# Kernel tuning notes

Hardware: AMD Instinct MI355X
Metric: run time of the kernel (lower is better)

## Reference

```python
import jax, jax.numpy as jnp
import numpy as np

F = 32          # num_features
E = 20          # size_of_expansion
CUTOFF = 5.0
N, K = 30000, 32  # nodes x dense neighbors


def cosine_cutoff(d, cutoff):
    # 0.5*(cos(pi*d/cutoff)+1) for d < cutoff, else 0
    return jnp.where(d < cutoff, 0.5 * (jnp.cos(jnp.pi * d / cutoff) + 1.0), 0.0)


def setup_inputs() -> dict:
    key = jax.random.key(0)
    ks = jax.random.split(key, 12)
    s = jax.random.normal(ks[0], (N, K, 1, F), jnp.float32)
    v = jax.random.normal(ks[1], (N, K, 3, F), jnp.float32)
    expansion = jax.random.normal(ks[2], (N, K, E), jnp.float32)
    direction = jax.random.normal(ks[3], (N, K, 3), jnp.float32)
    mask = (jax.random.uniform(ks[4], (N, K, 1)) > 0.2).astype(jnp.float32)
    edge_distance = jax.random.uniform(ks[5], (N, K, 1), jnp.float32) * (1.2 * CUTOFF)
    sc1 = 1.0 / np.sqrt(F)
    sc2 = 1.0 / np.sqrt(E)
    W1 = jax.random.uniform(ks[6], (F, F), jnp.float32, -sc1, sc1)
    b1 = jax.random.uniform(ks[7], (F,), jnp.float32, -sc1, sc1)
    W2 = jax.random.uniform(ks[8], (F, 3 * F), jnp.float32, -sc1, sc1)
    b2 = jax.random.uniform(ks[9], (3 * F,), jnp.float32, -sc1, sc1)
    Wr = jax.random.uniform(ks[10], (E, 3 * F), jnp.float32, -sc2, sc2)
    br = jax.random.uniform(ks[11], (3 * F,), jnp.float32, -sc2, sc2)
    return dict(s=s, v=v, expansion=expansion, direction=direction, mask=mask,
                edge_distance=edge_distance, W1=W1, b1=b1, W2=W2, b2=b2, Wr=Wr, br=br)


def reference(s, v, expansion, direction, mask, edge_distance, W1, b1, W2, b2, Wr, br):
    # msg_left: Linear -> SiLU -> Linear, on s [N,K,1,F] -> [N,K,1,3F]
    left_mul = jax.nn.silu(s @ W1 + b1) @ W2 + b2
    # msg_right: Linear on expansion [N,K,E] -> [N,K,3F] -> [N,K,1,3F]
    right_pre = (expansion @ Wr + br)[..., None, :]
    f_cut = cosine_cutoff(edge_distance, CUTOFF)[..., None]     # [N,K,1,1]
    gated = left_mul * (right_pre * f_cut)                      # [N,K,1,3F]
    a, b, c = jnp.split(gated, 3, axis=-1)                      # each [N,K,1,F]
    mask_ = mask[..., None]                                     # [N,K,1,1]
    delta_s = jnp.sum(mask_ * b, axis=-3)                       # [N,1,F]
    delta_v = jnp.sum(mask_ * (v * a + direction[..., None] * c), axis=-3)  # [N,3,F]
    return (delta_s, delta_v)
```

## Files before the change

kernel.cpp:

```cpp
#include <hip/hip_runtime.h>
#include <hip/hip_bf16.h>

typedef __attribute__((ext_vector_type(8))) short bf16x8;
typedef __attribute__((ext_vector_type(4))) float f32x4;

#define GSTR 68

__device__ __forceinline__ short f2bf(float f) {
  unsigned u = __float_as_uint(f);
  u += 0x7fffu + ((u >> 16) & 1u);
  return (short)(u >> 16);
}

__device__ __forceinline__ bf16x8 cvt8(float4 A, float4 B) {
  union { bf16x8 v; __hip_bfloat162 h[4]; } u;
  u.h[0] = __float22bfloat162_rn(make_float2(A.x, A.y));
  u.h[1] = __float22bfloat162_rn(make_float2(A.z, A.w));
  u.h[2] = __float22bfloat162_rn(make_float2(B.x, B.y));
  u.h[3] = __float22bfloat162_rn(make_float2(B.z, B.w));
  return u.v;
}

__device__ __forceinline__ bf16x8 ldsfrag(const int4* p) {
  union { int4 i; bf16x8 b; } u;
  u.i = *p;
  return u.b;
}

__device__ __forceinline__ float silu_(float x) {
  return __fdividef(x, 1.f + __expf(-x));
}

__global__ void pack_weights_kernel(
    const float* __restrict__ W1, const float* __restrict__ W2,
    const float* __restrict__ WR, const float* __restrict__ BR,
    int4* __restrict__ wsf)
{
  const int tid = threadIdx.x, wid = tid >> 6, l = tid & 63;
  const int col16 = l & 15, c = l >> 4, kc = c << 3;
  for (int t = wid; t < 14; t += 4) {
    int q[4];
    #pragma unroll
    for (int jj = 0; jj < 4; ++jj) {
      float f0, f1;
      if (t < 2) {
        int k0 = kc + 2*jj;
        int co = (t << 4) + col16;
        f0 = W1[k0*32 + co]; f1 = W1[(k0+1)*32 + co];
      } else if (t < 8) {
        int j0 = 2*jj;
        int feat = (j0 < 4) ? (4*c + j0) : (16 + 4*c + (j0 - 4));
        int co = ((t-2) << 4) + col16;
        f0 = W2[feat*96 + co]; f1 = W2[(feat+1)*96 + co];
      } else {
        int k0 = kc + 2*jj;
        int co = ((t-8) << 4) + col16;
        f0 = (k0   < 20) ? WR[k0*96 + co]     : ((k0   == 20) ? BR[co] : 0.f);
        f1 = (k0+1 < 20) ? WR[(k0+1)*96 + co] : ((k0+1 == 20) ? BR[co] : 0.f);
      }
      q[jj] = ((int)(unsigned short)f2bf(f0)) |
              (((int)(unsigned short)f2bf(f1)) << 16);
    }
    wsf[t*64 + l] = make_int4(q[0], q[1], q[2], q[3]);
  }
}

__global__ __launch_bounds__(256, 3) void deepdft_v9(
    const float* __restrict__ S, const float* __restrict__ V,
    const float* __restrict__ EXPN, const float* __restrict__ DIR,
    const float* __restrict__ MASK, const float* __restrict__ DIST,
    const float* __restrict__ B1, const float* __restrict__ B2,
    const int4* __restrict__ wsf,
    float* __restrict__ OUT, int n_nodes)
{
  __shared__ int4  wlds[14][64];
  __shared__ float glds[4][16 * GSTR];

  const int tid = threadIdx.x, wid = tid >> 6, l = tid & 63;
  const int col16 = l & 15, c = l >> 4, kc = c << 3;
  const int er8 = l >> 2, fo = l & 3;

  int n = blockIdx.x * 4 + wid;
  if (n >= n_nodes) n = n_nodes - 1;
  const int eb0 = n << 5, eb1 = eb0 + 16;

  float dv0 = DIST[eb0 + col16];
  float mv0 = MASK[eb0 + col16];
  float dv1 = DIST[eb1 + col16];
  float mv1 = MASK[eb1 + col16];
  float drv = DIR[(size_t)eb0 * 3 + (l < 48 ? l : 47)];

  #pragma unroll
  for (int t = wid; t < 14; t += 4) wlds[t][l] = wsf[t*64 + l];

  f32x4 b1a, b1b;
  {
    float4 t0 = *reinterpret_cast<const float4*>(B1 + 4*c);
    float4 t1 = *reinterpret_cast<const float4*>(B1 + 16 + 4*c);
    b1a[0]=t0.x; b1a[1]=t0.y; b1a[2]=t0.z; b1a[3]=t0.w;
    b1b[0]=t1.x; b1b[1]=t1.y; b1b[2]=t1.z; b1b[3]=t1.w;
  }
  float b2v[6];
  #pragma unroll
  for (int t = 0; t < 6; ++t) b2v[t] = B2[(t << 4) + col16];

  float wvl0 = 0.f, wvl1 = 0.f;
  if (dv0 < 5.f) wvl0 = mv0 * 0.5f * (__cosf(0.62831853071795865f * dv0) + 1.f);
  if (dv1 < 5.f) wvl1 = mv1 * 0.5f * (__cosf(0.62831853071795865f * dv1) + 1.f);

  const float4 z4 = make_float4(0.f, 0.f, 0.f, 0.f);
  float4 sS0 = z4, sS1 = z4, sE0 = z4;
  float4 sE1 = (c == 2) ? make_float4(1.f, 0.f, 0.f, 0.f) : z4;
  float4 vva[6];
  #pragma unroll
  for (int j = 0; j < 6; ++j) vva[j] = z4;

  auto issueS = [&](int eb) {
    const float* sp = S + (size_t)(eb + col16) * 32 + kc;
    sS0 = *reinterpret_cast<const float4*>(sp);
    sS1 = *reinterpret_cast<const float4*>(sp + 4);
    const float* ep = EXPN + (size_t)(eb + col16) * 20;
    if (c < 2) {
      sE0 = *reinterpret_cast<const float4*>(ep + kc);
      sE1 = *reinterpret_cast<const float4*>(ep + kc + 4);
    } else if (c == 2) {
      sE0 = *reinterpret_cast<const float4*>(ep + 16);
    }
  };
  auto issueV = [&](int eb) {
    const float* vb = V + (size_t)(eb + er8) * 96 + fo * 8;
    vva[0] = *reinterpret_cast<const float4*>(vb);
    vva[1] = *reinterpret_cast<const float4*>(vb + 4);
    vva[2] = *reinterpret_cast<const float4*>(vb + 32);
    vva[3] = *reinterpret_cast<const float4*>(vb + 36);
    vva[4] = *reinterpret_cast<const float4*>(vb + 64);
    vva[5] = *reinterpret_cast<const float4*>(vb + 68);
  };

  if (wvl0 != 0.f) issueS(eb0);
  {
    float wv_er = __shfl(wvl0, er8);
    if (wv_er != 0.f) issueV(eb0);
  }

  __syncthreads();

  float part[24];
  #pragma unroll
  for (int q = 0; q < 24; ++q) part[q] = 0.f;
  float accs0 = 0.f, accs1 = 0.f;
  float* gw = &glds[wid][0];
  const f32x4 z = {0.f, 0.f, 0.f, 0.f};

  #pragma unroll
  for (int it = 0; it < 2; ++it) {
    const float wvl = it ? wvl1 : wvl0;
    bf16x8 bs = cvt8(sS0, sS1);
    bf16x8 ae = cvt8(sE0, sE1);
    if (it == 0 && wvl1 != 0.f) issueS(eb1);

    f32x4 h0 = __builtin_amdgcn_mfma_f32_16x16x32_bf16(ldsfrag(&wlds[0][l]), bs, b1a, 0,0,0);
    f32x4 h1 = __builtin_amdgcn_mfma_f32_16x16x32_bf16(ldsfrag(&wlds[1][l]), bs, b1b, 0,0,0);
    bf16x8 ah;
    {
      union { bf16x8 v; __hip_bfloat162 h[4]; } u;
      u.h[0] = __float22bfloat162_rn(make_float2(silu_(h0[0]), silu_(h0[1])));
      u.h[1] = __float22bfloat162_rn(make_float2(silu_(h0[2]), silu_(h0[3])));
      u.h[2] = __float22bfloat162_rn(make_float2(silu_(h1[0]), silu_(h1[1])));
      u.h[3] = __float22bfloat162_rn(make_float2(silu_(h1[2]), silu_(h1[3])));
      ah = u.v;
    }

    float wv0 = __shfl(wvl, 4*c + 0);
    float wv1 = __shfl(wvl, 4*c + 1);
    float wv2 = __shfl(wvl, 4*c + 2);
    float wv3 = __shfl(wvl, 4*c + 3);

    #pragma unroll
    for (int tt = 0; tt < 2; ++tt) {
      f32x4 rA = __builtin_amdgcn_mfma_f32_16x16x32_bf16(ae, ldsfrag(&wlds[ 8+tt][l]), z, 0,0,0);
      f32x4 rB = __builtin_amdgcn_mfma_f32_16x16x32_bf16(ae, ldsfrag(&wlds[10+tt][l]), z, 0,0,0);
      f32x4 rC = __builtin_amdgcn_mfma_f32_16x16x32_bf16(ae, ldsfrag(&wlds[12+tt][l]), z, 0,0,0);
      f32x4 lA = __builtin_amdgcn_mfma_f32_16x16x32_bf16(ah, ldsfrag(&wlds[ 2+tt][l]), z, 0,0,0);
      f32x4 lB = __builtin_amdgcn_mfma_f32_16x16x32_bf16(ah, ldsfrag(&wlds[ 4+tt][l]), z, 0,0,0);
      f32x4 lC = __builtin_amdgcn_mfma_f32_16x16x32_bf16(ah, ldsfrag(&wlds[ 6+tt][l]), z, 0,0,0);
      #pragma unroll
      for (int r = 0; r < 4; ++r) {
        const float wv = (r==0) ? wv0 : (r==1) ? wv1 : (r==2) ? wv2 : wv3;
        const float ga = wv * (lA[r] + b2v[tt])   * rA[r];
        const float gb = wv * (lB[r] + b2v[2+tt]) * rB[r];
        const float gc = wv * (lC[r] + b2v[4+tt]) * rC[r];
        if (tt == 0) accs0 += gb; else accs1 += gb;
        *reinterpret_cast<float2*>(
            &gw[(4*c + r) * GSTR + 2*(col16 + 16*tt)]) = make_float2(ga, gc);
      }
    }
    __builtin_amdgcn_wave_barrier();

    float d0 = __shfl(drv, 3*er8 + 0);
    float d1 = __shfl(drv, 3*er8 + 1);
    float d2 = __shfl(drv, 3*er8 + 2);
    if (it == 0) drv = DIR[(size_t)eb1 * 3 + (l < 48 ? l : 47)];

    float4 gp[4];
    #pragma unroll
    for (int k = 0; k < 4; ++k)
      gp[k] = *reinterpret_cast<const float4*>(&gw[er8 * GSTR + 16*fo + 4*k]);

    #pragma unroll
    for (int ax = 0; ax < 3; ++ax) {
      const float dax = (ax==0) ? d0 : (ax==1) ? d1 : d2;
      #pragma unroll
      for (int j = 0; j < 8; ++j) {
        const float vj  = vva[2*ax + (j>>2)][j&3];
        const float gaj = gp[j>>1][(j&1)*2];
        const float gcj = gp[j>>1][(j&1)*2 + 1];
        part[ax*8+j] = fmaf(vj, gaj, fmaf(dax, gcj, part[ax*8+j]));
      }
    }
    if (it == 0) {
      float wv_er = __shfl(wvl1, er8);
      if (wv_er != 0.f) issueV(eb1);
    }
    __builtin_amdgcn_wave_barrier();
  }

  #pragma unroll
  for (int q = 0; q < 24; ++q) {
    part[q] += __shfl_xor(part[q], 4);
    part[q] += __shfl_xor(part[q], 8);
    part[q] += __shfl_xor(part[q], 16);
    part[q] += __shfl_xor(part[q], 32);
  }
  accs0 += __shfl_xor(accs0, 16); accs0 += __shfl_xor(accs0, 32);
  accs1 += __shfl_xor(accs1, 16); accs1 += __shfl_xor(accs1, 32);

  if (l < 16) {
    OUT[(size_t)n * 32 + col16]      = accs0;
    OUT[(size_t)n * 32 + 16 + col16] = accs1;
  }
  if (l < 4) {
    float* ov = OUT + (size_t)n_nodes * 32 + (size_t)n * 96 + 8*fo;
    #pragma unroll
    for (int ax = 0; ax < 3; ++ax) {
      *reinterpret_cast<float4*>(ov + ax*32) =
          make_float4(part[ax*8+0], part[ax*8+1], part[ax*8+2], part[ax*8+3]);
      *reinterpret_cast<float4*>(ov + ax*32 + 4) =
          make_float4(part[ax*8+4], part[ax*8+5], part[ax*8+6], part[ax*8+7]);
    }
  }
}

extern "C" void kernel_launch(void* const* d_in, const int* in_sizes, int n_in,
                              void* d_out, int out_size, void* d_ws, size_t ws_size,
                              hipStream_t stream) {
  const float* S    = (const float*)d_in[0];
  const float* V    = (const float*)d_in[1];
  const float* EXPN = (const float*)d_in[2];
  const float* DIR  = (const float*)d_in[3];
  const float* MASK = (const float*)d_in[4];
  const float* DIST = (const float*)d_in[5];
  const float* W1   = (const float*)d_in[6];
  const float* B1   = (const float*)d_in[7];
  const float* W2   = (const float*)d_in[8];
  const float* B2   = (const float*)d_in[9];
  const float* WR   = (const float*)d_in[10];
  const float* BR   = (const float*)d_in[11];
  float* OUT = (float*)d_out;
  int4* wsf = (int4*)d_ws;

  const int n_nodes = in_sizes[0] / 1024;
  const int grid = (n_nodes + 3) / 4;

  hipLaunchKernelGGL(pack_weights_kernel, dim3(1), dim3(256), 0, stream,
                     W1, W2, WR, BR, wsf);
  hipLaunchKernelGGL(deepdft_v9, dim3(grid), dim3(256), 0, stream,
                     S, V, EXPN, DIR, MASK, DIST, B1, B2, wsf, OUT, n_nodes);
}
```

Baseline: 109.2 us.

## Process two nodes per wave to amortize weight staging and prologue

Each wave now handles two consecutive nodes, which is four 16-edge iterations, and the grid shrinks by half. The per-block LDS weight load, bias loads and prologue are amortized over twice as many nodes, and prefetching of the next chunk's S/E/V/DIR data now continues across the node boundary. Distance and mask are loaded once for all 64 edges, and the cutoff weights are broadcast with shuffles. The cost is fewer blocks, which reduces parallelism and tail balance, and a longer serial chain per wave.

Result: slower. 206.1 us (+88.7%).

```diff
diff --git a/kernel.cpp b/kernel.cpp
--- a/kernel.cpp
+++ b/kernel.cpp
@@ -65,7 +65,7 @@
   }
 }
 
-__global__ __launch_bounds__(256, 3) void deepdft_v9(
+__global__ __launch_bounds__(256, 3) void deepdft_v10(
     const float* __restrict__ S, const float* __restrict__ V,
     const float* __restrict__ EXPN, const float* __restrict__ DIR,
     const float* __restrict__ MASK, const float* __restrict__ DIST,
@@ -80,15 +80,13 @@
   const int col16 = l & 15, c = l >> 4, kc = c << 3;
   const int er8 = l >> 2, fo = l & 3;
 
-  int n = blockIdx.x * 4 + wid;
-  if (n >= n_nodes) n = n_nodes - 1;
-  const int eb0 = n << 5, eb1 = eb0 + 16;
-
-  float dv0 = DIST[eb0 + col16];
-  float mv0 = MASK[eb0 + col16];
-  float dv1 = DIST[eb1 + col16];
-  float mv1 = MASK[eb1 + col16];
-  float drv = DIR[(size_t)eb0 * 3 + (l < 48 ? l : 47)];
+  int nb = blockIdx.x * 8 + wid * 2;
+  if (nb > n_nodes - 2) nb = (n_nodes >= 2) ? (n_nodes - 2) : 0;
+  const int ebase = nb << 5;
+
+  float dvA = DIST[ebase + l];
+  float mvA = MASK[ebase + l];
+  float drv = DIR[(size_t)ebase * 3 + (l < 48 ? l : 47)];
 
   #pragma unroll
   for (int t = wid; t < 14; t += 4) wlds[t][l] = wsf[t*64 + l];
@@ -104,9 +102,8 @@
   #pragma unroll
   for (int t = 0; t < 6; ++t) b2v[t] = B2[(t << 4) + col16];
 
-  float wvl0 = 0.f, wvl1 = 0.f;
-  if (dv0 < 5.f) wvl0 = mv0 * 0.5f * (__cosf(0.62831853071795865f * dv0) + 1.f);
-  if (dv1 < 5.f) wvl1 = mv1 * 0.5f * (__cosf(0.62831853071795865f * dv1) + 1.f);
+  float wvA = 0.f;
+  if (dvA < 5.f) wvA = mvA * 0.5f * (__cosf(0.62831853071795865f * dvA) + 1.f);
 
   const float4 z4 = make_float4(0.f, 0.f, 0.f, 0.f);
   float4 sS0 = z4, sS1 = z4, sE0 = z4;
@@ -137,11 +134,8 @@
     vva[5] = *reinterpret_cast<const float4*>(vb + 68);
   };
 
-  if (wvl0 != 0.f) issueS(eb0);
-  {
-    float wv_er = __shfl(wvl0, er8);
-    if (wv_er != 0.f) issueV(eb0);
-  }
+  { float p = __shfl(wvA, col16); if (p != 0.f) issueS(ebase); }
+  { float p = __shfl(wvA, er8);  if (p != 0.f) issueV(ebase); }
 
   __syncthreads();
 
@@ -153,11 +147,14 @@
   const f32x4 z = {0.f, 0.f, 0.f, 0.f};
 
   #pragma unroll
-  for (int it = 0; it < 2; ++it) {
-    const float wvl = it ? wvl1 : wvl0;
+  for (int it = 0; it < 4; ++it) {
+    const int ebn = ebase + ((it + 1) << 4);
     bf16x8 bs = cvt8(sS0, sS1);
     bf16x8 ae = cvt8(sE0, sE1);
-    if (it == 0 && wvl1 != 0.f) issueS(eb1);
+    if (it < 3) {
+      float p = __shfl(wvA, (it + 1) * 16 + col16);
+      if (p != 0.f) issueS(ebn);
+    }
 
     f32x4 h0 = __builtin_amdgcn_mfma_f32_16x16x32_bf16(ldsfrag(&wlds[0][l]), bs, b1a, 0,0,0);
     f32x4 h1 = __builtin_amdgcn_mfma_f32_16x16x32_bf16(ldsfrag(&wlds[1][l]), bs, b1b, 0,0,0);
@@ -171,10 +168,10 @@
       ah = u.v;
     }
 
-    float wv0 = __shfl(wvl, 4*c + 0);
-    float wv1 = __shfl(wvl, 4*c + 1);
-    float wv2 = __shfl(wvl, 4*c + 2);
-    float wv3 = __shfl(wvl, 4*c + 3);
+    float wv0 = __shfl(wvA, it * 16 + 4*c + 0);
+    float wv1 = __shfl(wvA, it * 16 + 4*c + 1);
+    float wv2 = __shfl(wvA, it * 16 + 4*c + 2);
+    float wv3 = __shfl(wvA, it * 16 + 4*c + 3);
 
     #pragma unroll
     for (int tt = 0; tt < 2; ++tt) {
@@ -200,7 +197,7 @@
     float d0 = __shfl(drv, 3*er8 + 0);
     float d1 = __shfl(drv, 3*er8 + 1);
     float d2 = __shfl(drv, 3*er8 + 2);
-    if (it == 0) drv = DIR[(size_t)eb1 * 3 + (l < 48 ? l : 47)];
+    if (it < 3) drv = DIR[(size_t)ebn * 3 + (l < 48 ? l : 47)];
 
     float4 gp[4];
     #pragma unroll
@@ -218,35 +215,43 @@
         part[ax*8+j] = fmaf(vj, gaj, fmaf(dax, gcj, part[ax*8+j]));
       }
     }
-    if (it == 0) {
-      float wv_er = __shfl(wvl1, er8);
-      if (wv_er != 0.f) issueV(eb1);
+    if (it < 3) {
+      float p = __shfl(wvA, (it + 1) * 16 + er8);
+      if (p != 0.f) issueV(ebn);
     }
     __builtin_amdgcn_wave_barrier();
-  }
-
-  #pragma unroll
-  for (int q = 0; q < 24; ++q) {
-    part[q] += __shfl_xor(part[q], 4);
-    part[q] += __shfl_xor(part[q], 8);
-    part[q] += __shfl_xor(part[q], 16);
-    part[q] += __shfl_xor(part[q], 32);
-  }
-  accs0 += __shfl_xor(accs0, 16); accs0 += __shfl_xor(accs0, 32);
-  accs1 += __shfl_xor(accs1, 16); accs1 += __shfl_xor(accs1, 32);
-
-  if (l < 16) {
-    OUT[(size_t)n * 32 + col16]      = accs0;
-    OUT[(size_t)n * 32 + 16 + col16] = accs1;
-  }
-  if (l < 4) {
-    float* ov = OUT + (size_t)n_nodes * 32 + (size_t)n * 96 + 8*fo;
-    #pragma unroll
-    for (int ax = 0; ax < 3; ++ax) {
-      *reinterpret_cast<float4*>(ov + ax*32) =
-          make_float4(part[ax*8+0], part[ax*8+1], part[ax*8+2], part[ax*8+3]);
-      *reinterpret_cast<float4*>(ov + ax*32 + 4) =
-          make_float4(part[ax*8+4], part[ax*8+5], part[ax*8+6], part[ax*8+7]);
+
+    if (it == 1 || it == 3) {
+      #pragma unroll
+      for (int q = 0; q < 24; ++q) {
+        part[q] += __shfl_xor(part[q], 4);
+        part[q] += __shfl_xor(part[q], 8);
+        part[q] += __shfl_xor(part[q], 16);
+        part[q] += __shfl_xor(part[q], 32);
+      }
+      accs0 += __shfl_xor(accs0, 16); accs0 += __shfl_xor(accs0, 32);
+      accs1 += __shfl_xor(accs1, 16); accs1 += __shfl_xor(accs1, 32);
+
+      const int node = nb + (it >> 1);
+      if (l < 16) {
+        OUT[(size_t)node * 32 + col16]      = accs0;
+        OUT[(size_t)node * 32 + 16 + col16] = accs1;
+      }
+      if (l < 4) {
+        float* ov = OUT + (size_t)n_nodes * 32 + (size_t)node * 96 + 8*fo;
+        #pragma unroll
+        for (int ax = 0; ax < 3; ++ax) {
+          *reinterpret_cast<float4*>(ov + ax*32) =
+              make_float4(part[ax*8+0], part[ax*8+1], part[ax*8+2], part[ax*8+3]);
+          *reinterpret_cast<float4*>(ov + ax*32 + 4) =
+              make_float4(part[ax*8+4], part[ax*8+5], part[ax*8+6], part[ax*8+7]);
+        }
+      }
+      if (it == 1) {
+        #pragma unroll
+        for (int q = 0; q < 24; ++q) part[q] = 0.f;
+        accs0 = 0.f; accs1 = 0.f;
+      }
     }
   }
 }
@@ -270,10 +275,10 @@
   int4* wsf = (int4*)d_ws;
 
   const int n_nodes = in_sizes[0] / 1024;
-  const int grid = (n_nodes + 3) / 4;
+  const int grid = (n_nodes + 7) / 8;
 
   hipLaunchKernelGGL(pack_weights_kernel, dim3(1), dim3(256), 0, stream,
                      W1, W2, WR, BR, wsf);
-  hipLaunchKernelGGL(deepdft_v9, dim3(grid), dim3(256), 0, stream,
+  hipLaunchKernelGGL(deepdft_v10, dim3(grid), dim3(256), 0, stream,
                      S, V, EXPN, DIR, MASK, DIST, B1, B2, wsf, OUT, n_nodes);
 }
```

## Load V directly into LDS via global_load_lds and consume gates in MFMA layout

Applied to the files above, without the earlier changes.

V tiles are now brought into a per-wave LDS buffer with global_load_lds (direct-to-LDS loads), and each load is skipped when the owning edge is masked or beyond the cutoff. Because V sits in LDS in the MFMA output layout, the gate values stay in registers and the LDS transpose of gates plus the large cross-lane shuffle reduction are no longer needed. The block-wide __syncthreads is removed and occupancy is raised to 4 blocks. In exchange the kernel relies on explicit waitcnt/sched barriers and must zero-fill the LDS buffer first so skipped rows read as zero.

Measured after the change: 186.5 us. 1.71x slower.

```diff
diff --git a/kernel.cpp b/kernel.cpp
--- a/kernel.cpp
+++ b/kernel.cpp
@@ -4,7 +4,8 @@
 typedef __attribute__((ext_vector_type(8))) short bf16x8;
 typedef __attribute__((ext_vector_type(4))) float f32x4;
 
-#define GSTR 68
+typedef const __attribute__((address_space(1))) unsigned int* gp1_t;
+typedef __attribute__((address_space(3))) unsigned int* lp3_t;
 
 __device__ __forceinline__ short f2bf(float f) {
   unsigned u = __float_as_uint(f);
@@ -65,7 +66,7 @@
   }
 }
 
-__global__ __launch_bounds__(256, 3) void deepdft_v9(
+__global__ __launch_bounds__(256, 4) void deepdft_v11(
     const float* __restrict__ S, const float* __restrict__ V,
     const float* __restrict__ EXPN, const float* __restrict__ DIR,
     const float* __restrict__ MASK, const float* __restrict__ DIST,
@@ -74,24 +75,18 @@
     float* __restrict__ OUT, int n_nodes)
 {
   __shared__ int4  wlds[14][64];
-  __shared__ float glds[4][16 * GSTR];
+  __shared__ float vbuf[4][1536];
 
   const int tid = threadIdx.x, wid = tid >> 6, l = tid & 63;
   const int col16 = l & 15, c = l >> 4, kc = c << 3;
-  const int er8 = l >> 2, fo = l & 3;
 
   int n = blockIdx.x * 4 + wid;
   if (n >= n_nodes) n = n_nodes - 1;
-  const int eb0 = n << 5, eb1 = eb0 + 16;
-
-  float dv0 = DIST[eb0 + col16];
-  float mv0 = MASK[eb0 + col16];
-  float dv1 = DIST[eb1 + col16];
-  float mv1 = MASK[eb1 + col16];
+  const int eb0 = n << 5;
+
+  float dv  = DIST[eb0 + (l & 31)];
+  float mv  = MASK[eb0 + (l & 31)];
   float drv = DIR[(size_t)eb0 * 3 + (l < 48 ? l : 47)];
-
-  #pragma unroll
-  for (int t = wid; t < 14; t += 4) wlds[t][l] = wsf[t*64 + l];
 
   f32x4 b1a, b1b;
   {
@@ -104,16 +99,26 @@
   #pragma unroll
   for (int t = 0; t < 6; ++t) b2v[t] = B2[(t << 4) + col16];
 
-  float wvl0 = 0.f, wvl1 = 0.f;
-  if (dv0 < 5.f) wvl0 = mv0 * 0.5f * (__cosf(0.62831853071795865f * dv0) + 1.f);
-  if (dv1 < 5.f) wvl1 = mv1 * 0.5f * (__cosf(0.62831853071795865f * dv1) + 1.f);
+  float* vb_lds = vbuf[wid];
+  {
+    const int4 zz = make_int4(0, 0, 0, 0);
+    #pragma unroll
+    for (int i = 0; i < 6; ++i)
+      *reinterpret_cast<int4*>(&vb_lds[i*256 + (l << 2)]) = zz;
+  }
+  asm volatile("s_waitcnt lgkmcnt(0)" ::: "memory");
+  __builtin_amdgcn_sched_barrier(0);
+
+  int e_[6];
+  #pragma unroll
+  for (int i = 0; i < 6; ++i) e_[i] = ((i << 6) + l) / 24;
+
+  float wvA = 0.f;
+  if (dv < 5.f) wvA = mv * 0.5f * (__cosf(0.62831853071795865f * dv) + 1.f);
 
   const float4 z4 = make_float4(0.f, 0.f, 0.f, 0.f);
   float4 sS0 = z4, sS1 = z4, sE0 = z4;
   float4 sE1 = (c == 2) ? make_float4(1.f, 0.f, 0.f, 0.f) : z4;
-  float4 vva[6];
-  #pragma unroll
-  for (int j = 0; j < 6; ++j) vva[j] = z4;
 
   auto issueS = [&](int eb) {
     const float* sp = S + (size_t)(eb + col16) * 32 + kc;
@@ -127,37 +132,31 @@
       sE0 = *reinterpret_cast<const float4*>(ep + 16);
     }
   };
-  auto issueV = [&](int eb) {
-    const float* vb = V + (size_t)(eb + er8) * 96 + fo * 8;
-    vva[0] = *reinterpret_cast<const float4*>(vb);
-    vva[1] = *reinterpret_cast<const float4*>(vb + 4);
-    vva[2] = *reinterpret_cast<const float4*>(vb + 32);
-    vva[3] = *reinterpret_cast<const float4*>(vb + 36);
-    vva[4] = *reinterpret_cast<const float4*>(vb + 64);
-    vva[5] = *reinterpret_cast<const float4*>(vb + 68);
+  auto issueV = [&](int eb, int hb) {
+    const float* Vb = V + (size_t)eb * 96;
+    #pragma unroll
+    for (int i = 0; i < 6; ++i) {
+      float p = __shfl(wvA, hb + e_[i]);
+      if (p != 0.f)
+        __builtin_amdgcn_global_load_lds(
+            (gp1_t)(Vb + i*256 + (l << 2)),
+            (lp3_t)(vb_lds + i*256), 16, 0, 0);
+    }
   };
 
-  if (wvl0 != 0.f) issueS(eb0);
-  {
-    float wv_er = __shfl(wvl0, er8);
-    if (wv_er != 0.f) issueV(eb0);
-  }
-
-  __syncthreads();
-
-  float part[24];
-  #pragma unroll
-  for (int q = 0; q < 24; ++q) part[q] = 0.f;
-  float accs0 = 0.f, accs1 = 0.f;
-  float* gw = &glds[wid][0];
+  { float p = __shfl(wvA, col16); if (p != 0.f) issueS(eb0); }
+  issueV(eb0, 0);
+
+  #pragma unroll
+  for (int t = 0; t < 14; ++t) wlds[t][l] = wsf[t*64 + l];
+
+  float acc[8] = {0.f,0.f,0.f,0.f,0.f,0.f,0.f,0.f};
   const f32x4 z = {0.f, 0.f, 0.f, 0.f};
 
   #pragma unroll
   for (int it = 0; it < 2; ++it) {
-    const float wvl = it ? wvl1 : wvl0;
     bf16x8 bs = cvt8(sS0, sS1);
     bf16x8 ae = cvt8(sE0, sE1);
-    if (it == 0 && wvl1 != 0.f) issueS(eb1);
 
     f32x4 h0 = __builtin_amdgcn_mfma_f32_16x16x32_bf16(ldsfrag(&wlds[0][l]), bs, b1a, 0,0,0);
     f32x4 h1 = __builtin_amdgcn_mfma_f32_16x16x32_bf16(ldsfrag(&wlds[1][l]), bs, b1b, 0,0,0);
@@ -171,11 +170,11 @@
       ah = u.v;
     }
 
-    float wv0 = __shfl(wvl, 4*c + 0);
-    float wv1 = __shfl(wvl, 4*c + 1);
-    float wv2 = __shfl(wvl, 4*c + 2);
-    float wv3 = __shfl(wvl, 4*c + 3);
-
+    float wvr[4];
+    #pragma unroll
+    for (int r = 0; r < 4; ++r) wvr[r] = __shfl(wvA, it*16 + 4*c + r);
+
+    float ga[2][4], gc[2][4];
     #pragma unroll
     for (int tt = 0; tt < 2; ++tt) {
       f32x4 rA = __builtin_amdgcn_mfma_f32_16x16x32_bf16(ae, ldsfrag(&wlds[ 8+tt][l]), z, 0,0,0);
@@ -186,68 +185,57 @@
       f32x4 lC = __builtin_amdgcn_mfma_f32_16x16x32_bf16(ah, ldsfrag(&wlds[ 6+tt][l]), z, 0,0,0);
       #pragma unroll
       for (int r = 0; r < 4; ++r) {
-        const float wv = (r==0) ? wv0 : (r==1) ? wv1 : (r==2) ? wv2 : wv3;
-        const float ga = wv * (lA[r] + b2v[tt])   * rA[r];
-        const float gb = wv * (lB[r] + b2v[2+tt]) * rB[r];
-        const float gc = wv * (lC[r] + b2v[4+tt]) * rC[r];
-        if (tt == 0) accs0 += gb; else accs1 += gb;
-        *reinterpret_cast<float2*>(
-            &gw[(4*c + r) * GSTR + 2*(col16 + 16*tt)]) = make_float2(ga, gc);
+        ga[tt][r] = wvr[r] * (lA[r] + b2v[tt])   * rA[r];
+        acc[tt]  += wvr[r] * (lB[r] + b2v[2+tt]) * rB[r];
+        gc[tt][r] = wvr[r] * (lC[r] + b2v[4+tt]) * rC[r];
       }
     }
-    __builtin_amdgcn_wave_barrier();
-
-    float d0 = __shfl(drv, 3*er8 + 0);
-    float d1 = __shfl(drv, 3*er8 + 1);
-    float d2 = __shfl(drv, 3*er8 + 2);
-    if (it == 0) drv = DIR[(size_t)eb1 * 3 + (l < 48 ? l : 47)];
-
-    float4 gp[4];
-    #pragma unroll
-    for (int k = 0; k < 4; ++k)
-      gp[k] = *reinterpret_cast<const float4*>(&gw[er8 * GSTR + 16*fo + 4*k]);
-
-    #pragma unroll
-    for (int ax = 0; ax < 3; ++ax) {
-      const float dax = (ax==0) ? d0 : (ax==1) ? d1 : d2;
+
+    float dax0[4], dax1[4], dax2[4];
+    #pragma unroll
+    for (int r = 0; r < 4; ++r) {
+      dax0[r] = __shfl(drv, 3*(4*c + r) + 0);
+      dax1[r] = __shfl(drv, 3*(4*c + r) + 1);
+      dax2[r] = __shfl(drv, 3*(4*c + r) + 2);
+    }
+
+    asm volatile("s_waitcnt vmcnt(0)" ::: "memory");
+    __builtin_amdgcn_sched_barrier(0);
+
+    #pragma unroll
+    for (int tt = 0; tt < 2; ++tt)
       #pragma unroll
-      for (int j = 0; j < 8; ++j) {
-        const float vj  = vva[2*ax + (j>>2)][j&3];
-        const float gaj = gp[j>>1][(j&1)*2];
-        const float gcj = gp[j>>1][(j&1)*2 + 1];
-        part[ax*8+j] = fmaf(vj, gaj, fmaf(dax, gcj, part[ax*8+j]));
+      for (int r = 0; r < 4; ++r) {
+        const int vb = (4*c + r)*96 + tt*16 + col16;
+        float v0 = vb_lds[vb];
+        float v1 = vb_lds[vb + 32];
+        float v2 = vb_lds[vb + 64];
+        acc[2+tt] = fmaf(v0, ga[tt][r], fmaf(dax0[r], gc[tt][r], acc[2+tt]));
+        acc[4+tt] = fmaf(v1, ga[tt][r], fmaf(dax1[r], gc[tt][r], acc[4+tt]));
+        acc[6+tt] = fmaf(v2, ga[tt][r], fmaf(dax2[r], gc[tt][r], acc[6+tt]));
       }
-    }
+
     if (it == 0) {
-      float wv_er = __shfl(wvl1, er8);
-      if (wv_er != 0.f) issueV(eb1);
-    }
-    __builtin_amdgcn_wave_barrier();
-  }
-
-  #pragma unroll
-  for (int q = 0; q < 24; ++q) {
-    part[q] += __shfl_xor(part[q], 4);
-    part[q] += __shfl_xor(part[q], 8);
-    part[q] += __shfl_xor(part[q], 16);
-    part[q] += __shfl_xor(part[q], 32);
-  }
-  accs0 += __shfl_xor(accs0, 16); accs0 += __shfl_xor(accs0, 32);
-  accs1 += __shfl_xor(accs1, 16); accs1 += __shfl_xor(accs1, 32);
-
+      asm volatile("s_waitcnt lgkmcnt(0)" ::: "memory");
+      __builtin_amdgcn_sched_barrier(0);
+      { float p = __shfl(wvA, 16 + col16); if (p != 0.f) issueS(eb0 + 16); }
+      issueV(eb0 + 16, 16);
+      drv = DIR[(size_t)(eb0 + 16) * 3 + (l < 48 ? l : 47)];
+    }
+  }
+
+  #pragma unroll
+  for (int q = 0; q < 8; ++q) {
+    acc[q] += __shfl_xor(acc[q], 16);
+    acc[q] += __shfl_xor(acc[q], 32);
+  }
   if (l < 16) {
-    OUT[(size_t)n * 32 + col16]      = accs0;
-    OUT[(size_t)n * 32 + 16 + col16] = accs1;
-  }
-  if (l < 4) {
-    float* ov = OUT + (size_t)n_nodes * 32 + (size_t)n * 96 + 8*fo;
-    #pragma unroll
-    for (int ax = 0; ax < 3; ++ax) {
-      *reinterpret_cast<float4*>(ov + ax*32) =
-          make_float4(part[ax*8+0], part[ax*8+1], part[ax*8+2], part[ax*8+3]);
-      *reinterpret_cast<float4*>(ov + ax*32 + 4) =
-          make_float4(part[ax*8+4], part[ax*8+5], part[ax*8+6], part[ax*8+7]);
-    }
+    OUT[(size_t)n * 32 + col16]      = acc[0];
+    OUT[(size_t)n * 32 + 16 + col16] = acc[1];
+    float* ov = OUT + (size_t)n_nodes * 32 + (size_t)n * 96;
+    ov[     col16] = acc[2]; ov[16 + col16] = acc[3];
+    ov[32 + col16] = acc[4]; ov[48 + col16] = acc[5];
+    ov[64 + col16] = acc[6]; ov[80 + col16] = acc[7];
   }
 }
 
@@ -274,6 +262,6 @@
 
   hipLaunchKernelGGL(pack_weights_kernel, dim3(1), dim3(256), 0, stream,
                      W1, W2, WR, BR, wsf);
-  hipLaunchKernelGGL(deepdft_v9, dim3(grid), dim3(256), 0, stream,
+  hipLaunchKernelGGL(deepdft_v11, dim3(grid), dim3(256), 0, stream,
                      S, V, EXPN, DIR, MASK, DIST, B1, B2, wsf, OUT, n_nodes);
 }
```
